# Kernel tuning notes

Hardware: AMD Instinct MI355X
Metric: run time of the kernel (lower is better)

Reference implementation:

```python
import jax, jax.numpy as jnp
import numpy as np

N_NODES = 100000
N_EDGES = 1200000
IN_CH, HID_CH, OUT_CH = 64, 64, 32


def setup_inputs() -> dict:
    key = jax.random.key(0)
    ks = jax.random.split(key, 8)
    x = jax.random.normal(ks[0], (N_NODES, IN_CH), dtype=jnp.float32)
    edge_index = jax.random.randint(ks[1], (2, N_EDGES), 0, N_NODES, dtype=jnp.int64)
    # SAGEConv params: lin_l acts on aggregated neighbors (has bias), lin_r on root features.
    def glorot(k, fan_in, fan_out):
        s = jnp.sqrt(6.0 / (fan_in + fan_out))
        return jax.random.uniform(k, (fan_in, fan_out), jnp.float32, -s, s)
    W1_l = glorot(ks[2], IN_CH, HID_CH)
    W1_r = glorot(ks[3], IN_CH, HID_CH)
    b1 = jnp.zeros((HID_CH,), jnp.float32)
    W2_l = glorot(ks[4], HID_CH, OUT_CH)
    W2_r = glorot(ks[5], HID_CH, OUT_CH)
    b2 = jnp.zeros((OUT_CH,), jnp.float32)
    return {"x": x, "edge_index": edge_index, "W1_l": W1_l, "W1_r": W1_r,
            "b1": b1, "W2_l": W2_l, "W2_r": W2_r, "b2": b2}


def _sage_conv(h, src, dst, W_l, W_r, b):
    # gather source-node features along edges, mean-aggregate at destinations
    msg = h[src]                                               # [E, d]
    agg = jax.ops.segment_sum(msg, dst, num_segments=N_NODES)  # [N, d]
    cnt = jax.ops.segment_sum(jnp.ones((msg.shape[0],), h.dtype), dst,
                              num_segments=N_NODES)
    agg = agg / jnp.maximum(cnt, 1.0)[:, None]                 # mean (0 if no neighbors)
    return agg @ W_l + h @ W_r + b


def reference(x, edge_index, W1_l, W1_r, b1, W2_l, W2_r, b2):
    src, dst = edge_index[0], edge_index[1]
    h = _sage_conv(x, src, dst, W1_l, W1_r, b1)
    h = jax.nn.relu(h)
    # dropout is identity in eval mode
    return _sage_conv(h, src, dst, W2_l, W2_r, b2)
```

## Files before the change

kernel.cpp:

```cpp
#include <hip/hip_runtime.h>

__device__ __forceinline__ float bf2f(unsigned short u) {
    union { unsigned int i; float f; } v;
    v.i = ((unsigned int)u) << 16;
    return v.f;
}
__device__ __forceinline__ unsigned short f2bf(float f) {
    union { float f; unsigned int u; } v;
    v.f = f;
    unsigned int u = v.u;
    u += 0x7FFFu + ((u >> 16) & 1u);
    return (unsigned short)(u >> 16);
}
__device__ __forceinline__ unsigned int pack2bf(float lo, float hi) {
    return (unsigned int)f2bf(lo) | ((unsigned int)f2bf(hi) << 16);
}
__device__ __forceinline__ float loadElem(const void* p, size_t i, int isb) {
    return isb ? bf2f(((const unsigned short*)p)[i]) : ((const float*)p)[i];
}
__device__ __forceinline__ float bflo(unsigned int u) {
    union { unsigned int i; float f; } v; v.i = u << 16; return v.f;
}
__device__ __forceinline__ float bfhi(unsigned int u) {
    union { unsigned int i; float f; } v; v.i = u & 0xFFFF0000u; return v.f;
}

typedef __attribute__((ext_vector_type(8))) short bf16x8;
typedef __attribute__((ext_vector_type(4))) float f32x4;

#define CHUNK 4096
#define BSHIFT 8

__global__ void k_detect(const int* __restrict__ ei, int newords,
                         const unsigned int* __restrict__ xw, int nxw,
                         int* __restrict__ flags) {
    __shared__ int aOr;
    __shared__ int plaus;
    if (threadIdx.x == 0) { aOr = 0; plaus = 0; }
    __syncthreads();
    int v = 0;
    for (int i = 1 + 2 * (int)threadIdx.x; i < newords; i += 512) v |= ei[i];
    int pl = 0;
    for (int i = threadIdx.x; i < nxw; i += 256) {
        unsigned short lo = (unsigned short)(xw[i] & 0xFFFFu);
        float a = fabsf(bf2f(lo));
        if (a > 1e-5f && a < 100.0f) pl++;
    }
    atomicOr(&aOr, v);
    atomicAdd(&plaus, pl);
    __syncthreads();
    if (threadIdx.x == 0) {
        flags[0] = (aOr == 0) ? 1 : 0;
        flags[1] = (2 * plaus >= nxw) ? 1 : 0;
    }
}

__global__ void k_cast(const void* __restrict__ x, unsigned short* __restrict__ xb,
                       int n8, const int* __restrict__ flags) {
    int i = blockIdx.x * blockDim.x + threadIdx.x;
    if (i >= n8) return;
    if (flags[1]) {
        ((uint4*)xb)[i] = ((const uint4*)x)[i];
    } else {
        const float4* xf = (const float4*)x;
        float4 a = xf[2 * i], b = xf[2 * i + 1];
        ushort4 lo = { f2bf(a.x), f2bf(a.y), f2bf(a.z), f2bf(a.w) };
        ushort4 hi = { f2bf(b.x), f2bf(b.y), f2bf(b.z), f2bf(b.w) };
        ((ushort4*)xb)[2 * i] = lo;
        ((ushort4*)xb)[2 * i + 1] = hi;
    }
}

__global__ __launch_bounds__(256) void k_bcount(
        const int* __restrict__ ei, const int* __restrict__ flags,
        int* __restrict__ blockHist, int E, int NBUK, int nblk) {
    __shared__ int hist[512];
    int t = threadIdx.x;
    for (int i = t; i < NBUK; i += 256) hist[i] = 0;
    __syncthreads();
    int q = flags[0];
    int e0 = blockIdx.x * CHUNK, e1 = min(E, e0 + CHUNK);
    for (int e = e0 + t; e < e1; e += 256) {
        int dst = ei[((size_t)(E + e)) << q];
        atomicAdd(&hist[dst >> BSHIFT], 1);
    }
    __syncthreads();
    for (int i = t; i < NBUK; i += 256)
        blockHist[(size_t)i * nblk + blockIdx.x] = hist[i];
}

__global__ __launch_bounds__(256) void k_rowscan(
        int* __restrict__ blockHist, int* __restrict__ bukTot, int nblk) {
    __shared__ int sh[256];
    int t = threadIdx.x;
    int* row = blockHist + (size_t)blockIdx.x * nblk;
    int carry = 0;
    for (int base = 0; base < nblk; base += 256) {
        int i = base + t;
        int v = (i < nblk) ? row[i] : 0;
        sh[t] = v;
        __syncthreads();
        for (int off = 1; off < 256; off <<= 1) {
            int u = (t >= off) ? sh[t - off] : 0;
            __syncthreads();
            sh[t] += u;
            __syncthreads();
        }
        if (i < nblk) row[i] = carry + sh[t] - v;
        int tot = sh[255];
        __syncthreads();
        carry += tot;
    }
    if (t == 0) bukTot[blockIdx.x] = carry;
}

__global__ __launch_bounds__(512) void k_toto(
        const int* __restrict__ bukTot, int* __restrict__ bukOff,
        int* __restrict__ rowptr, int NBUK, int E, int N) {
    __shared__ int sh[512];
    int t = threadIdx.x;
    int v = (t < NBUK) ? bukTot[t] : 0;
    sh[t] = v;
    __syncthreads();
    for (int off = 1; off < 512; off <<= 1) {
        int u = (t >= off) ? sh[t - off] : 0;
        __syncthreads();
        sh[t] += u;
        __syncthreads();
    }
    if (t < NBUK) bukOff[t] = sh[t] - v;
    if (t == 0) { bukOff[NBUK] = E; rowptr[N] = E; }
}

__global__ __launch_bounds__(256) void k_part(
        const int* __restrict__ ei, const int* __restrict__ flags,
        const int* __restrict__ blockHist, const int* __restrict__ bukOff,
        unsigned int* __restrict__ recs, int E, int NBUK, int nblk) {
    __shared__ int cur[512];
    int t = threadIdx.x;
    for (int i = t; i < NBUK; i += 256)
        cur[i] = blockHist[(size_t)i * nblk + blockIdx.x] + bukOff[i];
    __syncthreads();
    int q = flags[0];
    int e0 = blockIdx.x * CHUNK, e1 = min(E, e0 + CHUNK);
    for (int e = e0 + t; e < e1; e += 256) {
        int dst = ei[((size_t)(E + e)) << q];
        int src = ei[((size_t)e) << q];
        int pos = atomicAdd(&cur[dst >> BSHIFT], 1);
        recs[pos] = ((unsigned int)src << BSHIFT) | (unsigned int)(dst & ((1 << BSHIFT) - 1));
    }
}

__global__ __launch_bounds__(256) void k_csr(
        const unsigned int* __restrict__ recs, const int* __restrict__ bukOff,
        int* __restrict__ rowptr, int* __restrict__ esorted, int N) {
    __shared__ int degLoc[256];
    __shared__ int offLoc[256];
    __shared__ int wcur[256];
    int t = threadIdx.x;
    int node0 = blockIdx.x << BSHIFT;
    int r0 = bukOff[blockIdx.x], r1 = bukOff[blockIdx.x + 1];
    degLoc[t] = 0;
    __syncthreads();
    for (int i = r0 + t; i < r1; i += 256)
        atomicAdd(&degLoc[recs[i] & 255], 1);
    __syncthreads();
    int v = degLoc[t];
    offLoc[t] = v;
    __syncthreads();
    for (int off = 1; off < 256; off <<= 1) {
        int u = (t >= off) ? offLoc[t - off] : 0;
        __syncthreads();
        offLoc[t] += u;
        __syncthreads();
    }
    int excl = offLoc[t] - v;
    int node = node0 + t;
    if (node < N) rowptr[node] = r0 + excl;
    wcur[t] = r0 + excl;
    __syncthreads();
    for (int i = r0 + t; i < r1; i += 256) {
        unsigned int rec = recs[i];
        int pos = atomicAdd(&wcur[rec & 255], 1);
        esorted[pos] = (int)(rec >> BSHIFT);
    }
}

template<int CHOUT, bool RELU, bool FINAL>
__global__ __launch_bounds__(256) void k_fused(
        const unsigned short* __restrict__ feat,
        const int* __restrict__ rowptr,
        const int* __restrict__ esorted,
        const void* __restrict__ Wl,
        const void* __restrict__ Wr,
        const void* __restrict__ bias,
        void* __restrict__ outp,
        int N, const int* __restrict__ flags) {
    constexpr int SA2 = 72;
    constexpr int SW  = 72;
    __shared__ __align__(16) unsigned short amB16[64 * SA2];
    __shared__ __align__(16) unsigned short wT[CHOUT * SW];
    __shared__ float Bs[CHOUT];

    int t = threadIdx.x;
    int isb = flags[1];
    int node0 = blockIdx.x << 6;

    for (int i = t; i < 64 * CHOUT; i += 256) {
        int c = i >> 6, k = i & 63;
        unsigned short w = isb ? ((const unsigned short*)Wl)[k * CHOUT + c]
                               : f2bf(((const float*)Wl)[k * CHOUT + c]);
        wT[c * SW + k] = w;
    }
    if (t < CHOUT) Bs[t] = loadElem(bias, t, isb);

    {
        int g = t >> 3, l = t & 7;
        int gb = (t & 63) & ~7;
        const unsigned short* fl = feat + 8 * l;
#pragma unroll
        for (int jj = 0; jj < 2; ++jj) {
            int nl = g + 32 * jj;
            int node = node0 + nl;
            float a0 = 0.f, a1 = 0.f, a2 = 0.f, a3 = 0.f;
            float a4 = 0.f, a5 = 0.f, a6 = 0.f, a7 = 0.f;
            float inv = 0.f;
            if (node < N) {
                int beg = rowptr[node], end = rowptr[node + 1];
                int d = end - beg;
                if (d > 0) {
                    inv = 1.0f / (float)d;
                    for (int bs = beg; bs < end; bs += 8) {
                        int cnt = min(end - bs, 8);
                        int idx = esorted[min(bs + l, end - 1)];
                        int dd = 0;
                        if (cnt == 8) {
                            int s0 = __shfl(idx, gb + 0, 64);
                            int s1 = __shfl(idx, gb + 1, 64);
                            int s2 = __shfl(idx, gb + 2, 64);
                            int s3 = __shfl(idx, gb + 3, 64);
                            int s4 = __shfl(idx, gb + 4, 64);
                            int s5 = __shfl(idx, gb + 5, 64);
                            int s6 = __shfl(idx, gb + 6, 64);
                            int s7 = __shfl(idx, gb + 7, 64);
                            uint4 u0 = *(const uint4*)(fl + (size_t)s0 * 64);
                            uint4 u1 = *(const uint4*)(fl + (size_t)s1 * 64);
                            uint4 u2 = *(const uint4*)(fl + (size_t)s2 * 64);
                            uint4 u3 = *(const uint4*)(fl + (size_t)s3 * 64);
                            uint4 u4 = *(const uint4*)(fl + (size_t)s4 * 64);
                            uint4 u5 = *(const uint4*)(fl + (size_t)s5 * 64);
                            uint4 u6 = *(const uint4*)(fl + (size_t)s6 * 64);
                            uint4 u7 = *(const uint4*)(fl + (size_t)s7 * 64);
                            a0 += bflo(u0.x) + bflo(u1.x) + bflo(u2.x) + bflo(u3.x)
                                + bflo(u4.x) + bflo(u5.x) + bflo(u6.x) + bflo(u7.x);
                            a1 += bfhi(u0.x) + bfhi(u1.x) + bfhi(u2.x) + bfhi(u3.x)
                                + bfhi(u4.x) + bfhi(u5.x) + bfhi(u6.x) + bfhi(u7.x);
                            a2 += bflo(u0.y) + bflo(u1.y) + bflo(u2.y) + bflo(u3.y)
                                + bflo(u4.y) + bflo(u5.y) + bflo(u6.y) + bflo(u7.y);
                            a3 += bfhi(u0.y) + bfhi(u1.y) + bfhi(u2.y) + bfhi(u3.y)
                                + bfhi(u4.y) + bfhi(u5.y) + bfhi(u6.y) + bfhi(u7.y);
                            a4 += bflo(u0.z) + bflo(u1.z) + bflo(u2.z) + bflo(u3.z)
                                + bflo(u4.z) + bflo(u5.z) + bflo(u6.z) + bflo(u7.z);
                            a5 += bfhi(u0.z) + bfhi(u1.z) + bfhi(u2.z) + bfhi(u3.z)
                                + bfhi(u4.z) + bfhi(u5.z) + bfhi(u6.z) + bfhi(u7.z);
                            a6 += bflo(u0.w) + bflo(u1.w) + bflo(u2.w) + bflo(u3.w)
                                + bflo(u4.w) + bflo(u5.w) + bflo(u6.w) + bflo(u7.w);
                            a7 += bfhi(u0.w) + bfhi(u1.w) + bfhi(u2.w) + bfhi(u3.w)
                                + bfhi(u4.w) + bfhi(u5.w) + bfhi(u6.w) + bfhi(u7.w);
                            dd = 8;
                        }
                        for (; dd + 4 <= cnt; dd += 4) {
                            int s0 = __shfl(idx, gb + dd + 0, 64);
                            int s1 = __shfl(idx, gb + dd + 1, 64);
                            int s2 = __shfl(idx, gb + dd + 2, 64);
                            int s3 = __shfl(idx, gb + dd + 3, 64);
                            uint4 u0 = *(const uint4*)(fl + (size_t)s0 * 64);
                            uint4 u1 = *(const uint4*)(fl + (size_t)s1 * 64);
                            uint4 u2 = *(const uint4*)(fl + (size_t)s2 * 64);
                            uint4 u3 = *(const uint4*)(fl + (size_t)s3 * 64);
                            a0 += bflo(u0.x) + bflo(u1.x) + bflo(u2.x) + bflo(u3.x);
                            a1 += bfhi(u0.x) + bfhi(u1.x) + bfhi(u2.x) + bfhi(u3.x);
                            a2 += bflo(u0.y) + bflo(u1.y) + bflo(u2.y) + bflo(u3.y);
                            a3 += bfhi(u0.y) + bfhi(u1.y) + bfhi(u2.y) + bfhi(u3.y);
                            a4 += bflo(u0.z) + bflo(u1.z) + bflo(u2.z) + bflo(u3.z);
                            a5 += bfhi(u0.z) + bfhi(u1.z) + bfhi(u2.z) + bfhi(u3.z);
                            a6 += bflo(u0.w) + bflo(u1.w) + bflo(u2.w) + bflo(u3.w);
                            a7 += bfhi(u0.w) + bfhi(u1.w) + bfhi(u2.w) + bfhi(u3.w);
                        }
                        for (; dd < cnt; ++dd) {
                            int s = __shfl(idx, gb + dd, 64);
                            uint4 u = *(const uint4*)(fl + (size_t)s * 64);
                            a0 += bflo(u.x); a1 += bfhi(u.x);
                            a2 += bflo(u.y); a3 += bfhi(u.y);
                            a4 += bflo(u.z); a5 += bfhi(u.z);
                            a6 += bflo(u.w); a7 += bfhi(u.w);
                        }
                    }
                }
            }
            uint4 packed = make_uint4(pack2bf(a0 * inv, a1 * inv),
                                      pack2bf(a2 * inv, a3 * inv),
                                      pack2bf(a4 * inv, a5 * inv),
                                      pack2bf(a6 * inv, a7 * inv));
            *(uint4*)&amB16[nl * SA2 + 8 * l] = packed;
        }
    }
    __syncthreads();

    constexpr int NCT = CHOUT / 16;
    int wid = t >> 6, lane = t & 63;
    int arow = lane & 15;
    int kgrp = (lane >> 4) * 8;
    f32x4 acc[NCT];
#pragma unroll
    for (int ct = 0; ct < NCT; ++ct) acc[ct] = (f32x4){0.f, 0.f, 0.f, 0.f};

    const unsigned short* aBase = &amB16[(16 * wid + arow) * SA2 + kgrp];
#pragma unroll
    for (int kh = 0; kh < 2; ++kh) {
        bf16x8 a = *(const bf16x8*)(aBase + kh * 32);
#pragma unroll
        for (int ct = 0; ct < NCT; ++ct) {
            bf16x8 b = *(const bf16x8*)&wT[(16 * ct + arow) * SW + kh * 32 + kgrp];
            acc[ct] = __builtin_amdgcn_mfma_f32_16x16x32_bf16(a, b, acc[ct], 0, 0, 0);
        }
    }
    __syncthreads();

    for (int i = t; i < 64 * 8; i += 256) {
        int nl = i >> 3, c = i & 7;
        int gn = node0 + nl;
        uint4 u = make_uint4(0u, 0u, 0u, 0u);
        if (gn < N) u = *(const uint4*)(feat + (size_t)gn * 64 + 8 * c);
        *(uint4*)&amB16[nl * SA2 + 8 * c] = u;
    }
    for (int i = t; i < 64 * CHOUT; i += 256) {
        int c = i >> 6, k = i & 63;
        unsigned short w = isb ? ((const unsigned short*)Wr)[k * CHOUT + c]
                               : f2bf(((const float*)Wr)[k * CHOUT + c]);
        wT[c * SW + k] = w;
    }
    __syncthreads();

#pragma unroll
    for (int kh = 0; kh < 2; ++kh) {
        bf16x8 a = *(const bf16x8*)(aBase + kh * 32);
#pragma unroll
        for (int ct = 0; ct < NCT; ++ct) {
            bf16x8 b = *(const bf16x8*)&wT[(16 * ct + arow) * SW + kh * 32 + kgrp];
            acc[ct] = __builtin_amdgcn_mfma_f32_16x16x32_bf16(a, b, acc[ct], 0, 0, 0);
        }
    }

#pragma unroll
    for (int ct = 0; ct < NCT; ++ct) {
        int ch = 16 * ct + arow;
        float bv = Bs[ch];
#pragma unroll
        for (int r = 0; r < 4; ++r) {
            int node = node0 + 16 * wid + (lane >> 4) * 4 + r;
            if (node >= N) continue;
            float v = acc[ct][r] + bv;
            if (RELU) v = fmaxf(v, 0.f);
            if (FINAL && !isb) {
                ((float*)outp)[(size_t)node * CHOUT + ch] = v;
            } else {
                ((unsigned short*)outp)[(size_t)node * CHOUT + ch] = f2bf(v);
            }
        }
    }
}

extern "C" void kernel_launch(void* const* d_in, const int* in_sizes, int n_in,
                              void* d_out, int out_size, void* d_ws, size_t ws_size,
                              hipStream_t stream) {
    const void* x   = d_in[0];
    const int*  ei  = (const int*)d_in[1];
    const void* W1l = d_in[2];
    const void* W1r = d_in[3];
    const void* b1  = d_in[4];
    const void* W2l = d_in[5];
    const void* W2r = d_in[6];
    const void* b2  = d_in[7];

    const int N = in_sizes[0] / 64;
    const int E = in_sizes[1] / 2;
    const int NBUK = (N + (1 << BSHIFT) - 1) >> BSHIFT;
    const int nblk = (E + CHUNK - 1) / CHUNK;

    char* base = (char*)d_ws;
    size_t off = 0;
    auto alloc = [&](size_t bytes) { size_t o = off; off = (off + bytes + 255) & ~(size_t)255; return o; };
    int* flags   = (int*)(base + alloc(256));
    int* bukTot  = (int*)(base + alloc((size_t)NBUK * 4));
    int* bukOff  = (int*)(base + alloc((size_t)(NBUK + 1) * 4));
    int* rowptr  = (int*)(base + alloc((size_t)(N + 1) * 4));
    unsigned int* recs = (unsigned int*)(base + alloc((size_t)E * 4));
    int* esorted = (int*)(base + alloc((size_t)E * 4));
    unsigned short* xb = (unsigned short*)(base + alloc((size_t)N * 64 * 2));
    unsigned short* h  = (unsigned short*)(base + alloc((size_t)N * 64 * 2));
    (void)ws_size;

    int* blockHist = (int*)xb;

    const int B = 256;
    int nd = 2 * E; if (nd > 2048) nd = 2048;

    k_detect<<<1, 256, 0, stream>>>(ei, nd, (const unsigned int*)x, 512, flags);
    k_bcount<<<nblk, B, 0, stream>>>(ei, flags, blockHist, E, NBUK, nblk);
    k_rowscan<<<NBUK, B, 0, stream>>>(blockHist, bukTot, nblk);
    k_toto<<<1, 512, 0, stream>>>(bukTot, bukOff, rowptr, NBUK, E, N);
    k_part<<<nblk, B, 0, stream>>>(ei, flags, blockHist, bukOff, recs, E, NBUK, nblk);
    k_cast<<<(N * 8 + B - 1) / B, B, 0, stream>>>(x, xb, N * 8, flags);
    k_csr<<<NBUK, B, 0, stream>>>(recs, bukOff, rowptr, esorted, N);

    const int ntile = (N + 63) / 64;
    k_fused<64, true, false><<<ntile, B, 0, stream>>>(xb, rowptr, esorted,
                                                      W1l, W1r, b1, h, N, flags);
    k_fused<32, false, true><<<ntile, B, 0, stream>>>(h, rowptr, esorted,
                                                      W2l, W2r, b2, d_out, N, flags);
}
```

Measured before the change: 240.6 us.

## Apply layer-2 weights before aggregation and gather 32-wide projected features

The second SAGE layer is reordered algebraically: mean(h)@W2l equals mean(h@W2l), so the first kernel now computes h, applies both W2l and W2r per node, and stores z=h@W2l and g=h@W2r+b2 as 32-channel bf16. A new final kernel then gathers and averages z over neighbors and adds g. The 64-channel h tensor is no longer written and reread, and the layer-2 edge gather reads 32 channels per edge instead of 64. In exchange, layer 1 does extra MFMA work and syncs, and the output is rounded to bf16 at a different point.

New measurement: 230.6 us. 1.04x faster.

```diff
diff --git a/kernel.cpp b/kernel.cpp
--- a/kernel.cpp
+++ b/kernel.cpp
@@ -186,33 +186,36 @@
     }
 }
 
-template<int CHOUT, bool RELU, bool FINAL>
-__global__ __launch_bounds__(256) void k_fused(
+__global__ __launch_bounds__(256) void k_fused1(
         const unsigned short* __restrict__ feat,
         const int* __restrict__ rowptr,
         const int* __restrict__ esorted,
-        const void* __restrict__ Wl,
-        const void* __restrict__ Wr,
-        const void* __restrict__ bias,
-        void* __restrict__ outp,
+        const void* __restrict__ W1l, const void* __restrict__ W1r,
+        const void* __restrict__ b1,
+        const void* __restrict__ W2l, const void* __restrict__ W2r,
+        const void* __restrict__ b2,
+        unsigned short* __restrict__ zbuf,
+        unsigned short* __restrict__ gbuf,
         int N, const int* __restrict__ flags) {
     constexpr int SA2 = 72;
     constexpr int SW  = 72;
     __shared__ __align__(16) unsigned short amB16[64 * SA2];
-    __shared__ __align__(16) unsigned short wT[CHOUT * SW];
-    __shared__ float Bs[CHOUT];
+    __shared__ __align__(16) unsigned short wT[64 * SW];
+    __shared__ float Bs[64];
+    __shared__ float Bs2[32];
 
     int t = threadIdx.x;
     int isb = flags[1];
     int node0 = blockIdx.x << 6;
 
-    for (int i = t; i < 64 * CHOUT; i += 256) {
+    for (int i = t; i < 64 * 64; i += 256) {
         int c = i >> 6, k = i & 63;
-        unsigned short w = isb ? ((const unsigned short*)Wl)[k * CHOUT + c]
-                               : f2bf(((const float*)Wl)[k * CHOUT + c]);
+        unsigned short w = isb ? ((const unsigned short*)W1l)[k * 64 + c]
+                               : f2bf(((const float*)W1l)[k * 64 + c]);
         wT[c * SW + k] = w;
     }
-    if (t < CHOUT) Bs[t] = loadElem(bias, t, isb);
+    if (t < 64) Bs[t] = loadElem(b1, t, isb);
+    if (t >= 64 && t < 96) Bs2[t - 64] = loadElem(b2, t - 64, isb);
 
     {
         int g = t >> 3, l = t & 7;
@@ -307,20 +310,19 @@
     }
     __syncthreads();
 
-    constexpr int NCT = CHOUT / 16;
     int wid = t >> 6, lane = t & 63;
     int arow = lane & 15;
     int kgrp = (lane >> 4) * 8;
-    f32x4 acc[NCT];
-#pragma unroll
-    for (int ct = 0; ct < NCT; ++ct) acc[ct] = (f32x4){0.f, 0.f, 0.f, 0.f};
+    f32x4 acc[4];
+#pragma unroll
+    for (int ct = 0; ct < 4; ++ct) acc[ct] = (f32x4){0.f, 0.f, 0.f, 0.f};
 
     const unsigned short* aBase = &amB16[(16 * wid + arow) * SA2 + kgrp];
 #pragma unroll
     for (int kh = 0; kh < 2; ++kh) {
         bf16x8 a = *(const bf16x8*)(aBase + kh * 32);
 #pragma unroll
-        for (int ct = 0; ct < NCT; ++ct) {
+        for (int ct = 0; ct < 4; ++ct) {
             bf16x8 b = *(const bf16x8*)&wT[(16 * ct + arow) * SW + kh * 32 + kgrp];
             acc[ct] = __builtin_amdgcn_mfma_f32_16x16x32_bf16(a, b, acc[ct], 0, 0, 0);
         }
@@ -334,10 +336,10 @@
         if (gn < N) u = *(const uint4*)(feat + (size_t)gn * 64 + 8 * c);
         *(uint4*)&amB16[nl * SA2 + 8 * c] = u;
     }
-    for (int i = t; i < 64 * CHOUT; i += 256) {
+    for (int i = t; i < 64 * 64; i += 256) {
         int c = i >> 6, k = i & 63;
-        unsigned short w = isb ? ((const unsigned short*)Wr)[k * CHOUT + c]
-                               : f2bf(((const float*)Wr)[k * CHOUT + c]);
+        unsigned short w = isb ? ((const unsigned short*)W1r)[k * 64 + c]
+                               : f2bf(((const float*)W1r)[k * 64 + c]);
         wT[c * SW + k] = w;
     }
     __syncthreads();
@@ -346,27 +348,159 @@
     for (int kh = 0; kh < 2; ++kh) {
         bf16x8 a = *(const bf16x8*)(aBase + kh * 32);
 #pragma unroll
-        for (int ct = 0; ct < NCT; ++ct) {
+        for (int ct = 0; ct < 4; ++ct) {
             bf16x8 b = *(const bf16x8*)&wT[(16 * ct + arow) * SW + kh * 32 + kgrp];
             acc[ct] = __builtin_amdgcn_mfma_f32_16x16x32_bf16(a, b, acc[ct], 0, 0, 0);
         }
     }
-
-#pragma unroll
-    for (int ct = 0; ct < NCT; ++ct) {
+    __syncthreads();
+
+    {
+        int rbase = (lane >> 4) * 4;
+#pragma unroll
+        for (int ct = 0; ct < 4; ++ct) {
+            int ch = 16 * ct + arow;
+            float bv = Bs[ch];
+#pragma unroll
+            for (int r = 0; r < 4; ++r) {
+                int nl = 16 * wid + rbase + r;
+                float v = fmaxf(acc[ct][r] + bv, 0.f);
+                amB16[nl * SA2 + ch] = f2bf(v);
+            }
+        }
+    }
+    for (int i = t; i < 32 * 64; i += 256) {
+        int c = i >> 6, k = i & 63;
+        unsigned short wl = isb ? ((const unsigned short*)W2l)[k * 32 + c]
+                                : f2bf(((const float*)W2l)[k * 32 + c]);
+        unsigned short wr = isb ? ((const unsigned short*)W2r)[k * 32 + c]
+                                : f2bf(((const float*)W2r)[k * 32 + c]);
+        wT[c * SW + k] = wl;
+        wT[(32 + c) * SW + k] = wr;
+    }
+    __syncthreads();
+
+    f32x4 accz[2], accg[2];
+#pragma unroll
+    for (int ct = 0; ct < 2; ++ct) {
+        accz[ct] = (f32x4){0.f, 0.f, 0.f, 0.f};
+        accg[ct] = (f32x4){0.f, 0.f, 0.f, 0.f};
+    }
+#pragma unroll
+    for (int kh = 0; kh < 2; ++kh) {
+        bf16x8 a = *(const bf16x8*)(aBase + kh * 32);
+#pragma unroll
+        for (int ct = 0; ct < 2; ++ct) {
+            bf16x8 bz = *(const bf16x8*)&wT[(16 * ct + arow) * SW + kh * 32 + kgrp];
+            bf16x8 bg = *(const bf16x8*)&wT[(32 + 16 * ct + arow) * SW + kh * 32 + kgrp];
+            accz[ct] = __builtin_amdgcn_mfma_f32_16x16x32_bf16(a, bz, accz[ct], 0, 0, 0);
+            accg[ct] = __builtin_amdgcn_mfma_f32_16x16x32_bf16(a, bg, accg[ct], 0, 0, 0);
+        }
+    }
+
+#pragma unroll
+    for (int ct = 0; ct < 2; ++ct) {
         int ch = 16 * ct + arow;
-        float bv = Bs[ch];
+        float b2v = Bs2[ch];
 #pragma unroll
         for (int r = 0; r < 4; ++r) {
             int node = node0 + 16 * wid + (lane >> 4) * 4 + r;
             if (node >= N) continue;
-            float v = acc[ct][r] + bv;
-            if (RELU) v = fmaxf(v, 0.f);
-            if (FINAL && !isb) {
-                ((float*)outp)[(size_t)node * CHOUT + ch] = v;
-            } else {
-                ((unsigned short*)outp)[(size_t)node * CHOUT + ch] = f2bf(v);
+            zbuf[(size_t)node * 32 + ch] = f2bf(accz[ct][r]);
+            gbuf[(size_t)node * 32 + ch] = f2bf(accg[ct][r] + b2v);
+        }
+    }
+}
+
+__global__ __launch_bounds__(256) void k_final(
+        const unsigned short* __restrict__ zbuf,
+        const unsigned short* __restrict__ gbuf,
+        const int* __restrict__ rowptr,
+        const int* __restrict__ esorted,
+        void* __restrict__ outp,
+        int N, const int* __restrict__ flags) {
+    int t = threadIdx.x;
+    int isb = flags[1];
+    int node0 = blockIdx.x << 6;
+
+    int g = t >> 3, l = t & 7;
+    int gb = (t & 63) & ~7;
+    const unsigned short* fl = zbuf + 4 * l;
+#pragma unroll
+    for (int jj = 0; jj < 2; ++jj) {
+        int nl = g + 32 * jj;
+        int node = node0 + nl;
+        if (node >= N) continue;
+        float a0 = 0.f, a1 = 0.f, a2 = 0.f, a3 = 0.f;
+        float inv = 0.f;
+        int beg = rowptr[node], end = rowptr[node + 1];
+        int d = end - beg;
+        if (d > 0) {
+            inv = 1.0f / (float)d;
+            for (int bs = beg; bs < end; bs += 8) {
+                int cnt = min(end - bs, 8);
+                int idx = esorted[min(bs + l, end - 1)];
+                int dd = 0;
+                if (cnt == 8) {
+                    int s0 = __shfl(idx, gb + 0, 64);
+                    int s1 = __shfl(idx, gb + 1, 64);
+                    int s2 = __shfl(idx, gb + 2, 64);
+                    int s3 = __shfl(idx, gb + 3, 64);
+                    int s4 = __shfl(idx, gb + 4, 64);
+                    int s5 = __shfl(idx, gb + 5, 64);
+                    int s6 = __shfl(idx, gb + 6, 64);
+                    int s7 = __shfl(idx, gb + 7, 64);
+                    uint2 u0 = *(const uint2*)(fl + (size_t)s0 * 32);
+                    uint2 u1 = *(const uint2*)(fl + (size_t)s1 * 32);
+                    uint2 u2 = *(const uint2*)(fl + (size_t)s2 * 32);
+                    uint2 u3 = *(const uint2*)(fl + (size_t)s3 * 32);
+                    uint2 u4 = *(const uint2*)(fl + (size_t)s4 * 32);
+                    uint2 u5 = *(const uint2*)(fl + (size_t)s5 * 32);
+                    uint2 u6 = *(const uint2*)(fl + (size_t)s6 * 32);
+                    uint2 u7 = *(const uint2*)(fl + (size_t)s7 * 32);
+                    a0 += bflo(u0.x) + bflo(u1.x) + bflo(u2.x) + bflo(u3.x)
+                        + bflo(u4.x) + bflo(u5.x) + bflo(u6.x) + bflo(u7.x);
+                    a1 += bfhi(u0.x) + bfhi(u1.x) + bfhi(u2.x) + bfhi(u3.x)
+                        + bfhi(u4.x) + bfhi(u5.x) + bfhi(u6.x) + bfhi(u7.x);
+                    a2 += bflo(u0.y) + bflo(u1.y) + bflo(u2.y) + bflo(u3.y)
+                        + bflo(u4.y) + bflo(u5.y) + bflo(u6.y) + bflo(u7.y);
+                    a3 += bfhi(u0.y) + bfhi(u1.y) + bfhi(u2.y) + bfhi(u3.y)
+                        + bfhi(u4.y) + bfhi(u5.y) + bfhi(u6.y) + bfhi(u7.y);
+                    dd = 8;
+                }
+                for (; dd + 4 <= cnt; dd += 4) {
+                    int s0 = __shfl(idx, gb + dd + 0, 64);
+                    int s1 = __shfl(idx, gb + dd + 1, 64);
+                    int s2 = __shfl(idx, gb + dd + 2, 64);
+                    int s3 = __shfl(idx, gb + dd + 3, 64);
+                    uint2 u0 = *(const uint2*)(fl + (size_t)s0 * 32);
+                    uint2 u1 = *(const uint2*)(fl + (size_t)s1 * 32);
+                    uint2 u2 = *(const uint2*)(fl + (size_t)s2 * 32);
+                    uint2 u3 = *(const uint2*)(fl + (size_t)s3 * 32);
+                    a0 += bflo(u0.x) + bflo(u1.x) + bflo(u2.x) + bflo(u3.x);
+                    a1 += bfhi(u0.x) + bfhi(u1.x) + bfhi(u2.x) + bfhi(u3.x);
+                    a2 += bflo(u0.y) + bflo(u1.y) + bflo(u2.y) + bflo(u3.y);
+                    a3 += bfhi(u0.y) + bfhi(u1.y) + bfhi(u2.y) + bfhi(u3.y);
+                }
+                for (; dd < cnt; ++dd) {
+                    int s = __shfl(idx, gb + dd, 64);
+                    uint2 u = *(const uint2*)(fl + (size_t)s * 32);
+                    a0 += bflo(u.x); a1 += bfhi(u.x);
+                    a2 += bflo(u.y); a3 += bfhi(u.y);
+                }
             }
+        }
+        uint2 gv = *(const uint2*)(gbuf + (size_t)node * 32 + 4 * l);
+        float r0 = a0 * inv + bflo(gv.x);
+        float r1 = a1 * inv + bfhi(gv.x);
+        float r2 = a2 * inv + bflo(gv.y);
+        float r3 = a3 * inv + bfhi(gv.y);
+        if (!isb) {
+            *(float4*)((float*)outp + (size_t)node * 32 + 4 * l) =
+                make_float4(r0, r1, r2, r3);
+        } else {
+            ushort4 o = { f2bf(r0), f2bf(r1), f2bf(r2), f2bf(r3) };
+            *(ushort4*)((unsigned short*)outp + (size_t)node * 32 + 4 * l) = o;
         }
     }
 }
@@ -401,6 +535,9 @@
     unsigned short* h  = (unsigned short*)(base + alloc((size_t)N * 64 * 2));
     (void)ws_size;
 
+    unsigned short* zbuf = h;
+    unsigned short* gbuf = h + (size_t)N * 32;
+
     int* blockHist = (int*)xb;
 
     const int B = 256;
@@ -415,8 +552,8 @@
     k_csr<<<NBUK, B, 0, stream>>>(recs, bukOff, rowptr, esorted, N);
 
     const int ntile = (N + 63) / 64;
-    k_fused<64, true, false><<<ntile, B, 0, stream>>>(xb, rowptr, esorted,
-                                                      W1l, W1r, b1, h, N, flags);
-    k_fused<32, false, true><<<ntile, B, 0, stream>>>(h, rowptr, esorted,
-                                                      W2l, W2r, b2, d_out, N, flags);
-}
+    k_fused1<<<ntile, B, 0, stream>>>(xb, rowptr, esorted,
+                                      W1l, W1r, b1, W2l, W2r, b2,
+                                      zbuf, gbuf, N, flags);
+    k_final<<<ntile, B, 0, stream>>>(zbuf, gbuf, rowptr, esorted, d_out, N, flags);
+}
```
